# Optimization experiments

Measured on AMD Instinct MI355X. Metric: run time of the kernel, lower is better.

Reference implementation:

```python
import jax, jax.numpy as jnp
import numpy as np
from jax import lax

DT = 1.0  # self.dt


def setup_inputs() -> dict:
    key = jax.random.key(0)
    k1, k2 = jax.random.split(key)
    B, T, D = 16, 4096, 512
    x = jax.random.normal(k1, (B, T, D), dtype=jnp.float32)
    W = jax.random.normal(k2, (D,), dtype=jnp.float32)  # CustomLinearLayer.weight
    return {"x": x, "W": W}


def reference(x, W):
    # w = exp(-exp(W)) - 1 in (-1, 0]; w_res = sqrt(1 - w^2)
    w = jnp.exp(-jnp.exp(W)) - 1.0          # [D]
    w_res = jnp.sqrt(1.0 - w * w)           # [D]
    a = 1.0 + DT * w                        # decay factor per channel, [D]
    b = DT * w_res                          # input scale per channel, [D]

    # h_{t+1} = h_t + dt * (h_t * w + x_t * w_res) = a * h_t + b * x_t
    bx = x * b                              # [B, T, D] (fused elementwise)
    xt = jnp.swapaxes(bx, 0, 1)             # [T, B, D] scan over time

    def step(h, u):
        h_next = a * h + u
        return h_next, h_next

    h0 = jnp.zeros(x.shape[:1] + x.shape[2:], dtype=x.dtype)  # [B, D]
    _, hs = lax.scan(step, h0, xt)          # hs: [T, B, D]
    return jnp.swapaxes(hs, 0, 1)           # [B, T, D] (return_sequences=True)
```

## Files before the change

kernel.cpp:

```cpp
#include <hip/hip_runtime.h>


#define BB 16
#define TT 4096
#define DD 512
#define KK 128
#define LL (TT / KK)
#define D4 (DD / 4)
#define LBN 12

typedef float vfloat4 __attribute__((ext_vector_type(4)));

__device__ __forceinline__ void coeffs(const float* __restrict__ W, int d4,
                                       vfloat4& a, vfloat4& bs, vfloat4& a32) {
    const vfloat4 wv = ((const vfloat4*)W)[d4];
    a.x = expf(-expf(wv.x)); a.y = expf(-expf(wv.y));
    a.z = expf(-expf(wv.z)); a.w = expf(-expf(wv.w));
    const vfloat4 w1 = a - 1.0f;
    bs.x = sqrtf(1.0f - w1.x * w1.x); bs.y = sqrtf(1.0f - w1.y * w1.y);
    bs.z = sqrtf(1.0f - w1.z * w1.z); bs.w = sqrtf(1.0f - w1.w * w1.w);
    a32 = a;
#pragma unroll
    for (int i = 0; i < 5; ++i) a32 *= a32;
}

__global__ __launch_bounds__(256) void lru_p1(const vfloat4* __restrict__ x,
                                              const float* __restrict__ W,
                                              vfloat4* __restrict__ E) {
    const int d4 = threadIdx.x;
    const int k  = blockIdx.x * 2 + threadIdx.y;
    const int b  = blockIdx.y;

    vfloat4 a, bs, a32;
    coeffs(W, d4, a, bs, a32);

    const vfloat4* xp = x + ((size_t)b * TT + (size_t)k * LL) * D4 + d4;
    vfloat4 h = {0.f, 0.f, 0.f, 0.f};
#pragma unroll
    for (int i = 0; i < LL; ++i) {
        vfloat4 v = xp[(size_t)i * D4];
        h = a * h + bs * v;
    }
    E[((size_t)b * KK + k) * D4 + d4] = h;
}

__global__ __launch_bounds__(256) void lru_p2(const vfloat4* __restrict__ x,
                                              const float* __restrict__ W,
                                              const vfloat4* __restrict__ E,
                                              vfloat4* __restrict__ out) {
    const int d4 = threadIdx.x;
    const int k  = blockIdx.x * 2 + threadIdx.y;
    const int b  = blockIdx.y;

    vfloat4 a, bs, a32;
    coeffs(W, d4, a, bs, a32);

    const int nlb = (k < LBN) ? k : LBN;
    const size_t erow = (size_t)b * KK * D4 + d4;
    vfloat4 c = {0.f, 0.f, 0.f, 0.f};
    vfloat4 m = {1.f, 1.f, 1.f, 1.f};
    for (int j = 1; j <= nlb; ++j) {
        c = c + m * E[erow + (size_t)(k - j) * D4];
        m = m * a32;
    }

    const size_t base = ((size_t)b * TT + (size_t)k * LL) * D4 + d4;
    const vfloat4* xp = x + base;
    vfloat4* op = (vfloat4*)(out + base);
    vfloat4 h = c;
#pragma unroll
    for (int i = 0; i < LL; ++i) {
        vfloat4 v = xp[(size_t)i * D4];
        h = a * h + bs * v;
        __builtin_nontemporal_store(h, &op[(size_t)i * D4]);
    }
}

extern "C" void kernel_launch(void* const* d_in, const int* in_sizes, int n_in,
                              void* d_out, int out_size, void* d_ws, size_t ws_size,
                              hipStream_t stream) {
    const vfloat4* x = (const vfloat4*)d_in[0];
    const float*   W = (const float*)d_in[1];
    vfloat4* out = (vfloat4*)d_out;

    vfloat4* E = (vfloat4*)d_ws;

    dim3 grid(KK / 2, BB);
    dim3 block(D4, 2);
    lru_p1<<<grid, block, 0, stream>>>(x, W, E);
    lru_p2<<<grid, block, 0, stream>>>(x, W, E, out);
}
```

Before: 252.6 us.

## Fuse two-pass chunked scan into single kernel with recomputed history

Replaces the two-kernel chunk scan (local end states then lookback) with one kernel where each block recomputes a 384-step history from x in three parallel groups, combines them in shared memory with a^128 powers, and then scans its 256-step tile in two groups. This removes the workspace round trip and the second launch. In exchange it reads x redundantly for the history and uses fewer, longer serial chains per thread.

```diff
diff --git a/kernel.cpp b/kernel.cpp
--- a/kernel.cpp
+++ b/kernel.cpp
@@ -4,75 +4,63 @@
 #define BB 16
 #define TT 4096
 #define DD 512
-#define KK 128
-#define LL (TT / KK)
 #define D4 (DD / 4)
-#define LBN 12
+#define TILE 256
+#define HIST 384
+#define GL 128
+#define NG 5
+#define NTL (TT / TILE)
 
 typedef float vfloat4 __attribute__((ext_vector_type(4)));
 
-__device__ __forceinline__ void coeffs(const float* __restrict__ W, int d4,
-                                       vfloat4& a, vfloat4& bs, vfloat4& a32) {
+__global__ __launch_bounds__(640) void lru_fused(const vfloat4* __restrict__ x,
+                                                 const float* __restrict__ W,
+                                                 vfloat4* __restrict__ out) {
+    __shared__ vfloat4 sE[4][D4];
+
+    const int d4 = threadIdx.x;
+    const int g  = threadIdx.y;
+    const int k  = blockIdx.x;
+    const int b  = blockIdx.y;
+
     const vfloat4 wv = ((const vfloat4*)W)[d4];
+    vfloat4 a;
     a.x = expf(-expf(wv.x)); a.y = expf(-expf(wv.y));
     a.z = expf(-expf(wv.z)); a.w = expf(-expf(wv.w));
     const vfloat4 w1 = a - 1.0f;
+    vfloat4 bs;
     bs.x = sqrtf(1.0f - w1.x * w1.x); bs.y = sqrtf(1.0f - w1.y * w1.y);
     bs.z = sqrtf(1.0f - w1.z * w1.z); bs.w = sqrtf(1.0f - w1.w * w1.w);
-    a32 = a;
+    vfloat4 a128 = a;
 #pragma unroll
-    for (int i = 0; i < 5; ++i) a32 *= a32;
-}
+    for (int i = 0; i < 7; ++i) a128 *= a128;
 
-__global__ __launch_bounds__(256) void lru_p1(const vfloat4* __restrict__ x,
-                                              const float* __restrict__ W,
-                                              vfloat4* __restrict__ E) {
-    const int d4 = threadIdx.x;
-    const int k  = blockIdx.x * 2 + threadIdx.y;
-    const int b  = blockIdx.y;
+    const int r0 = k * TILE - HIST + g * GL;
+    const vfloat4* xp = x + (((size_t)b * TT + r0) * D4 + d4);
 
-    vfloat4 a, bs, a32;
-    coeffs(W, d4, a, bs, a32);
+    vfloat4 h = {0.f, 0.f, 0.f, 0.f};
+    if (g < 4 && r0 >= 0) {
+#pragma unroll 8
+        for (int i = 0; i < GL; ++i) {
+            vfloat4 v = xp[(size_t)i * D4];
+            h = a * h + bs * v;
+        }
+    }
+    if (g < 4) sE[g][d4] = h;
+    __syncthreads();
+    if (g < 3) return;
 
-    const vfloat4* xp = x + ((size_t)b * TT + (size_t)k * LL) * D4 + d4;
-    vfloat4 h = {0.f, 0.f, 0.f, 0.f};
-#pragma unroll
-    for (int i = 0; i < LL; ++i) {
+    vfloat4 S = sE[0][d4];
+    S = sE[1][d4] + a128 * S;
+    S = sE[2][d4] + a128 * S;
+    if (g == 4) S = sE[3][d4] + a128 * S;
+
+    vfloat4* op = out + (((size_t)b * TT + r0) * D4 + d4);
+#pragma unroll 8
+    for (int i = 0; i < GL; ++i) {
         vfloat4 v = xp[(size_t)i * D4];
-        h = a * h + bs * v;
-    }
-    E[((size_t)b * KK + k) * D4 + d4] = h;
-}
-
-__global__ __launch_bounds__(256) void lru_p2(const vfloat4* __restrict__ x,
-                                              const float* __restrict__ W,
-                                              const vfloat4* __restrict__ E,
-                                              vfloat4* __restrict__ out) {
-    const int d4 = threadIdx.x;
-    const int k  = blockIdx.x * 2 + threadIdx.y;
-    const int b  = blockIdx.y;
-
-    vfloat4 a, bs, a32;
-    coeffs(W, d4, a, bs, a32);
-
-    const int nlb = (k < LBN) ? k : LBN;
-    const size_t erow = (size_t)b * KK * D4 + d4;
-    vfloat4 c = {0.f, 0.f, 0.f, 0.f};
-    vfloat4 m = {1.f, 1.f, 1.f, 1.f};
-    for (int j = 1; j <= nlb; ++j) {
-        c = c + m * E[erow + (size_t)(k - j) * D4];
-        m = m * a32;
-    }
-
-    const size_t base = ((size_t)b * TT + (size_t)k * LL) * D4 + d4;
-    const vfloat4* xp = x + base;
-    vfloat4* op = (vfloat4*)(out + base);
-    vfloat4 h = c;
-#pragma unroll
-    for (int i = 0; i < LL; ++i) {
-        vfloat4 v = xp[(size_t)i * D4];
-        h = a * h + bs * v;
-        __builtin_nontemporal_store(h, &op[(size_t)i * D4]);
+        S = a * S + bs * v;
+        __builtin_nontemporal_store(S, &op[(size_t)i * D4]);
     }
 }
 
@@ -83,10 +71,7 @@
     const float*   W = (const float*)d_in[1];
     vfloat4* out = (vfloat4*)d_out;
 
-    vfloat4* E = (vfloat4*)d_ws;
-
-    dim3 grid(KK / 2, BB);
-    dim3 block(D4, 2);
-    lru_p1<<<grid, block, 0, stream>>>(x, W, E);
-    lru_p2<<<grid, block, 0, stream>>>(x, W, E, out);
+    dim3 grid(NTL, BB);
+    dim3 block(D4, NG);
+    lru_fused<<<grid, block, 0, stream>>>(x, W, out);
 }
```

After: 260.2 us. 3.0% more time.
